# Kernel tuning notes

Hardware: AMD Instinct MI355X
Metric: run time of the kernel (lower is better)

## Reference

```python
import jax, jax.numpy as jnp
import numpy as np

B, H, L, D = 2, 16, 2048, 128


def setup_inputs() -> dict:
    key = jax.random.key(0)
    kq, kk, kv = jax.random.split(key, 3)
    q = jax.random.normal(kq, (B, H, L, D), dtype=jnp.float32)
    k = jax.random.normal(kk, (B, H, L, D), dtype=jnp.float32)
    v = jax.random.normal(kv, (B, H, L, D), dtype=jnp.float32)
    return {"q": q, "k": k, "v": v}


def reference(q, k, v):
    # Causal prefill attention (flash_attn_varlen_func / SDPA is_causal=True path).
    # q, k, v: [B, H, L, D]; scale = 1/sqrt(D) as in the fallback and constructor.
    Lq = q.shape[2]
    Dh = q.shape[3]
    scale = 1.0 / jnp.sqrt(jnp.asarray(Dh, q.dtype))
    scores = jnp.einsum('bhqd,bhkd->bhqk', q, k) * scale  # [B,H,Lq,Lk]
    causal = jnp.tril(jnp.ones((Lq, Lq), dtype=bool))      # [Lq,Lk]
    scores = jnp.where(causal, scores, jnp.finfo(q.dtype).min)
    probs = jax.nn.softmax(scores, axis=-1)
    return jnp.einsum('bhqk,bhkd->bhqd', probs, v)          # [B,H,Lq,D]
```

## Files before the change

kernel.cpp:

```cpp
#include <hip/hip_runtime.h>
#include <hip/hip_bf16.h>
#include <stdint.h>


#define BB 2
#define HH 16
#define LL 2048
#define DD 128

typedef float f32x4 __attribute__((ext_vector_type(4)));
typedef __bf16 bf16x8 __attribute__((ext_vector_type(8)));

union Frag16 {
    uint4    u;
    bf16x8   b;
    uint16_t s[8];
    uint32_t w32[4];
};

__device__ inline uint32_t pk2bf(float x, float y) {
    uint32_t ux = __builtin_bit_cast(uint32_t, x);
    uint32_t uy = __builtin_bit_cast(uint32_t, y);
    ux += 0x7fffu + ((ux >> 16) & 1u);
    uy += 0x7fffu + ((uy >> 16) & 1u);
    return (ux >> 16) | (uy & 0xffff0000u);
}

__device__ inline uint16_t f2bf(float x) {
    uint32_t u = __builtin_bit_cast(uint32_t, x);
    u += 0x7fffu + ((u >> 16) & 1u);
    return (uint16_t)(u >> 16);
}

__global__ __launch_bounds__(256) void conv_all(
    const float* __restrict__ Qg, const float* __restrict__ Kg,
    const float* __restrict__ Vg,
    uint4* __restrict__ Qf, uint4* __restrict__ Kf, uint4* __restrict__ Vf)
{
    const int bid = blockIdx.x;
    const int t   = threadIdx.x;
    if (bid < 4096) {
        const bool isK = bid >= 2048;
        const int  unit = isK ? bid - 2048 : bid;
        const float* src = isK ? Kg : Qg;
        uint4*       dst = isK ? Kf : Qf;
        #pragma unroll
        for (int i = 0; i < 2; ++i) {
            const int local = t + i * 256;
            const int tile  = unit * 2 + (local >> 8);
            const int c     = local & 255;
            const int ds = c >> 6, quad = (c >> 4) & 3, n16 = c & 15;
            const float* p = src + ((size_t)tile * 16 + n16) * DD + ds * 32 + quad * 8;
            float4 a = *(const float4*)p;
            float4 b = *(const float4*)(p + 4);
            Frag16 f;
            f.w32[0] = pk2bf(a.x, a.y); f.w32[1] = pk2bf(a.z, a.w);
            f.w32[2] = pk2bf(b.x, b.y); f.w32[3] = pk2bf(b.z, b.w);
            dst[(size_t)tile * 256 + c] = f.u;
        }
    } else {
        const int g = bid - 4096;
        const int n16 = t & 15, dt = (t >> 4) & 7, quadH = t >> 7;
        #pragma unroll
        for (int qi = 0; qi < 2; ++qi) {
            const int quad = quadH + 2 * qi;
            const float* base = Vg + ((size_t)g * 32 + quad * 8) * DD + dt * 16 + n16;
            float v[8];
            #pragma unroll
            for (int j = 0; j < 8; ++j) v[j] = base[(size_t)j * DD];
            Frag16 f;
            f.w32[0] = pk2bf(v[0], v[1]); f.w32[1] = pk2bf(v[2], v[3]);
            f.w32[2] = pk2bf(v[4], v[5]); f.w32[3] = pk2bf(v[6], v[7]);
            Vf[(size_t)g * 512 + dt * 64 + quad * 16 + n16] = f.u;
        }
    }
}

__global__ __launch_bounds__(256, 2) void fa_main(
    const uint4* __restrict__ Qf, const uint4* __restrict__ Kf,
    const uint4* __restrict__ Vf, float* __restrict__ Og)
{
    __shared__ __align__(16) uint16_t Plds[4][16 * 72];

    const int tid  = threadIdx.x;
    const int lane = tid & 63;
    const int w    = tid >> 6;
    const int n16  = lane & 15;
    const int quad = lane >> 4;

    const int i    = blockIdx.x;
    const int xcd  = i & 7;
    const int rest = i >> 3;
    const int bh   = xcd * 4 + (rest >> 4);
    const int pair = rest & 15;

    constexpr float kC   = 0.08838834764831845f * 1.4426950408889634f;
    constexpr float kOff = -16.0f * 1.4426950408889634f;

    const uint4* kpb = Kf + (size_t)(bh * 128) * 256 + lane;
    const uint4* vpb = Vf + (size_t)(bh * 64) * 512 + lane;
    float* Oh = Og + (size_t)bh * LL * DD;

    #pragma unroll
    for (int phase = 0; phase < 2; ++phase) {
        const int qtile  = phase ? pair : 31 - pair;
        const int q0     = qtile * 64;
        const int q_base = q0 + w * 16;

        Frag16 qf[4];
        {
            const uint4* qp = Qf + ((size_t)(bh * 128 + (q_base >> 4)) * 256) + lane;
            #pragma unroll
            for (int ds = 0; ds < 4; ++ds) qf[ds].u = qp[ds * 64];
        }

        f32x4 oacc[8];
        #pragma unroll
        for (int dt = 0; dt < 8; ++dt) oacc[dt] = (f32x4)0.0f;
        float lpart = 0.0f;

        const int ntiles = (q0 >> 6) + 1;

        for (int t = 0; t < ntiles; ++t) {
            const int kv0 = t << 6;
            const uint4* kp = kpb + (size_t)(kv0 >> 4) * 256;
            const uint4* vp = vpb + (size_t)(kv0 >> 5) * 512;

            f32x4 sacc[4] = {(f32x4)0.0f, (f32x4)0.0f, (f32x4)0.0f, (f32x4)0.0f};
            {
                Frag16 kf[2][4];
                #pragma unroll
                for (int kt = 0; kt < 2; ++kt)
                    #pragma unroll
                    for (int ds = 0; ds < 4; ++ds) kf[kt][ds].u = kp[kt * 256 + ds * 64];
                #pragma unroll
                for (int ds = 0; ds < 4; ++ds) {
                    sacc[0] = __builtin_amdgcn_mfma_f32_16x16x32_bf16(kf[0][ds].b, qf[ds].b, sacc[0], 0, 0, 0);
                    sacc[1] = __builtin_amdgcn_mfma_f32_16x16x32_bf16(kf[1][ds].b, qf[ds].b, sacc[1], 0, 0, 0);
                }
                #pragma unroll
                for (int kt = 0; kt < 2; ++kt)
                    #pragma unroll
                    for (int ds = 0; ds < 4; ++ds) kf[kt][ds].u = kp[(kt + 2) * 256 + ds * 64];
                #pragma unroll
                for (int ds = 0; ds < 4; ++ds) {
                    sacc[2] = __builtin_amdgcn_mfma_f32_16x16x32_bf16(kf[0][ds].b, qf[ds].b, sacc[2], 0, 0, 0);
                    sacc[3] = __builtin_amdgcn_mfma_f32_16x16x32_bf16(kf[1][ds].b, qf[ds].b, sacc[3], 0, 0, 0);
                }
            }

            Frag16 vf[2][8];
            #pragma unroll
            for (int h = 0; h < 2; ++h)
                #pragma unroll
                for (int dt = 0; dt < 8; ++dt) vf[h][dt].u = vp[h * 512 + dt * 64];

            if (kv0 + 63 > q_base) {
                const int qg_ = q_base + n16;
                #pragma unroll
                for (int kt = 0; kt < 4; ++kt) {
                    const int kvg = kv0 + kt * 16 + quad * 4;
                    #pragma unroll
                    for (int r = 0; r < 4; ++r)
                        if (kvg + r > qg_) sacc[kt][r] = -1e30f;
                }
            }

            #pragma unroll
            for (int kt = 0; kt < 4; ++kt) {
                float p0 = exp2f(fmaf(sacc[kt][0], kC, kOff));
                float p1 = exp2f(fmaf(sacc[kt][1], kC, kOff));
                float p2 = exp2f(fmaf(sacc[kt][2], kC, kOff));
                float p3 = exp2f(fmaf(sacc[kt][3], kC, kOff));
                lpart += (p0 + p1) + (p2 + p3);
                uint2 pw;
                pw.x = pk2bf(p0, p1);
                pw.y = pk2bf(p2, p3);
                *(uint2*)&Plds[w][n16 * 72 + kt * 16 + quad * 4] = pw;
            }

            #pragma unroll
            for (int h = 0; h < 2; ++h) {
                Frag16 pf;
                pf.u = *(const uint4*)&Plds[w][n16 * 72 + h * 32 + quad * 8];
                #pragma unroll
                for (int dt = 0; dt < 8; ++dt)
                    oacc[dt] = __builtin_amdgcn_mfma_f32_16x16x32_bf16(
                        pf.b, vf[h][dt].b, oacc[dt], 0, 0, 0);
            }
        }

        float lsum = lpart;
        lsum += __shfl_xor(lsum, 16);
        lsum += __shfl_xor(lsum, 32);
        #pragma unroll
        for (int r = 0; r < 4; ++r) {
            const float inv = 1.0f / __shfl(lsum, quad * 4 + r);
            float* orow = Oh + (size_t)(q_base + quad * 4 + r) * DD + n16;
            #pragma unroll
            for (int dt = 0; dt < 8; ++dt)
                orow[dt * 16] = oacc[dt][r] * inv;
        }
    }
}

__global__ __launch_bounds__(256) void fa_fallback(
    const float* __restrict__ Qg, const float* __restrict__ Kg,
    const float* __restrict__ Vg, float* __restrict__ Og)
{
    __shared__ uint4 Klds[32 * 16];
    __shared__ uint4 Vlds[128 * 4];
    __shared__ __align__(16) uint16_t Plds[4][32 * 40];

    const int tid  = threadIdx.x;
    const int lane = tid & 63;
    const int w    = tid >> 6;
    const int n16  = lane & 15;
    const int quad = lane >> 4;

    const int bh     = blockIdx.y;
    const int q0     = (gridDim.x - 1 - blockIdx.x) * 128;
    const int q_base = q0 + w * 32;

    const size_t base = (size_t)bh * LL * DD;
    const float* Qh = Qg + base;
    const float* Kh = Kg + base;
    const float* Vh = Vg + base;
    float*       Oh = Og + base;

    constexpr float kC = 0.08838834764831845f * 1.4426950408889634f;

    Frag16 qf[2][4];
    #pragma unroll
    for (int qt = 0; qt < 2; ++qt) {
        const float* qrow = Qh + (size_t)(q_base + qt * 16 + n16) * DD;
        #pragma unroll
        for (int ds = 0; ds < 4; ++ds) {
            const int d0 = ds * 32 + quad * 8;
            float4 a = *(const float4*)(qrow + d0);
            float4 b = *(const float4*)(qrow + d0 + 4);
            Frag16 f;
            f.s[0] = f2bf(a.x); f.s[1] = f2bf(a.y); f.s[2] = f2bf(a.z); f.s[3] = f2bf(a.w);
            f.s[4] = f2bf(b.x); f.s[5] = f2bf(b.y); f.s[6] = f2bf(b.z); f.s[7] = f2bf(b.w);
            qf[qt][ds] = f;
        }
    }

    f32x4 oacc[2][8];
    #pragma unroll
    for (int qt = 0; qt < 2; ++qt)
        #pragma unroll
        for (int dt = 0; dt < 8; ++dt) oacc[qt][dt] = (f32x4)0.0f;
    float mrow[2] = {-1e30f, -1e30f};
    float lrow[2] = {0.0f, 0.0f};

    const int ntiles = q0 / 32 + 4;

    for (int t = 0; t < ntiles; ++t) {
        const int kv0 = t * 32;
        __syncthreads();
        #pragma unroll
        for (int iu = 0; iu < 2; ++iu) {
            const int cid = tid + iu * 256;
            const int r = cid >> 4, c = cid & 15;
            const float* src = Kh + (size_t)(kv0 + r) * DD + c * 8;
            float4 a = *(const float4*)src;
            float4 b = *(const float4*)(src + 4);
            Frag16 f;
            f.s[0] = f2bf(a.x); f.s[1] = f2bf(a.y); f.s[2] = f2bf(a.z); f.s[3] = f2bf(a.w);
            f.s[4] = f2bf(b.x); f.s[5] = f2bf(b.y); f.s[6] = f2bf(b.z); f.s[7] = f2bf(b.w);
            Klds[r * 16 + (c ^ (r & 7))] = f.u;
        }
        #pragma unroll
        for (int iu = 0; iu < 2; ++iu) {
            const int cid = tid + iu * 256;
            const int d = cid >> 2, ch = cid & 3;
            const float* src = Vh + (size_t)(kv0 + ch * 8) * DD + d;
            Frag16 f;
            #pragma unroll
            for (int j = 0; j < 8; ++j) f.s[j] = f2bf(src[(size_t)j * DD]);
            Vlds[d * 4 + (ch ^ ((d >> 1) & 3))] = f.u;
        }
        __syncthreads();

        if (kv0 > q_base + 31) continue;

        f32x4 sacc[2][2];
        #pragma unroll
        for (int kt = 0; kt < 2; ++kt)
            #pragma unroll
            for (int qt = 0; qt < 2; ++qt) sacc[kt][qt] = (f32x4)0.0f;

        #pragma unroll
        for (int ds = 0; ds < 4; ++ds) {
            Frag16 kfr[2];
            #pragma unroll
            for (int kt = 0; kt < 2; ++kt) {
                const int r = kt * 16 + n16;
                const int c = ds * 4 + quad;
                kfr[kt].u = Klds[r * 16 + (c ^ (r & 7))];
            }
            #pragma unroll
            for (int kt = 0; kt < 2; ++kt)
                #pragma unroll
                for (int qt = 0; qt < 2; ++qt)
                    sacc[kt][qt] = __builtin_amdgcn_mfma_f32_16x16x32_bf16(
                        kfr[kt].b, qf[qt][ds].b, sacc[kt][qt], 0, 0, 0);
        }

        if (kv0 + 31 > q_base) {
            #pragma unroll
            for (int kt = 0; kt < 2; ++kt) {
                const int kvg = kv0 + kt * 16 + quad * 4;
                #pragma unroll
                for (int qt = 0; qt < 2; ++qt) {
                    const int qg_ = q_base + qt * 16 + n16;
                    #pragma unroll
                    for (int r = 0; r < 4; ++r)
                        if (kvg + r > qg_) sacc[kt][qt][r] = -1e30f;
                }
            }
        }

        #pragma unroll
        for (int qt = 0; qt < 2; ++qt) {
            float mt = sacc[0][qt][0];
            #pragma unroll
            for (int kt = 0; kt < 2; ++kt)
                #pragma unroll
                for (int r = 0; r < 4; ++r) mt = fmaxf(mt, sacc[kt][qt][r]);
            mt = fmaxf(mt, __shfl_xor(mt, 16));
            mt = fmaxf(mt, __shfl_xor(mt, 32));
            const float mnew  = fmaxf(mrow[qt], mt);
            const float alpha = exp2f((mrow[qt] - mnew) * kC);
            mrow[qt] = mnew;

            float ls = 0.0f;
            uint16_t* prow = &Plds[w][(qt * 16 + n16) * 40];
            #pragma unroll
            for (int kt = 0; kt < 2; ++kt)
                #pragma unroll
                for (int r = 0; r < 4; ++r) {
                    const float p = exp2f((sacc[kt][qt][r] - mnew) * kC);
                    ls += p;
                    prow[kt * 16 + quad * 4 + r] = f2bf(p);
                }
            ls += __shfl_xor(ls, 16);
            ls += __shfl_xor(ls, 32);
            lrow[qt] = lrow[qt] * alpha + ls;

            #pragma unroll
            for (int r = 0; r < 4; ++r) {
                const float ar = __shfl(alpha, quad * 4 + r);
                #pragma unroll
                for (int dt = 0; dt < 8; ++dt) oacc[qt][dt][r] *= ar;
            }
        }

        Frag16 pfr[2];
        #pragma unroll
        for (int qt = 0; qt < 2; ++qt)
            pfr[qt].u = *(const uint4*)&Plds[w][(qt * 16 + n16) * 40 + quad * 8];
        #pragma unroll
        for (int dt = 0; dt < 8; ++dt) {
            const int d = dt * 16 + n16;
            Frag16 vfr;
            vfr.u = Vlds[d * 4 + (quad ^ ((d >> 1) & 3))];
            #pragma unroll
            for (int qt = 0; qt < 2; ++qt)
                oacc[qt][dt] = __builtin_amdgcn_mfma_f32_16x16x32_bf16(
                    pfr[qt].b, vfr.b, oacc[qt][dt], 0, 0, 0);
        }
    }

    #pragma unroll
    for (int qt = 0; qt < 2; ++qt) {
        #pragma unroll
        for (int r = 0; r < 4; ++r) {
            const float lr  = __shfl(lrow[qt], quad * 4 + r);
            const float inv = 1.0f / lr;
            const int row = q_base + qt * 16 + quad * 4 + r;
            float* orow = Oh + (size_t)row * DD + n16;
            #pragma unroll
            for (int dt = 0; dt < 8; ++dt)
                orow[dt * 16] = oacc[qt][dt][r] * inv;
        }
    }
}

extern "C" void kernel_launch(void* const* d_in, const int* in_sizes, int n_in,
                              void* d_out, int out_size, void* d_ws, size_t ws_size,
                              hipStream_t stream) {
    const float* q = (const float*)d_in[0];
    const float* k = (const float*)d_in[1];
    const float* v = (const float*)d_in[2];
    float* o = (float*)d_out;

    const size_t TENS = (size_t)BB * HH * LL * DD * 2;
    if (ws_size >= 3 * TENS) {
        uint4* Qf = (uint4*)d_ws;
        uint4* Kf = (uint4*)((char*)d_ws + TENS);
        uint4* Vf = (uint4*)((char*)d_ws + 2 * TENS);
        conv_all<<<dim3(6144), dim3(256), 0, stream>>>(q, k, v, Qf, Kf, Vf);
        fa_main<<<dim3(512), dim3(256), 0, stream>>>(Qf, Kf, Vf, o);
    } else {
        fa_fallback<<<dim3(16, BB * HH), dim3(256), 0, stream>>>(q, k, v, o);
    }
}
```

Measured before the change: 206.1 us.

## Split KV range across warps per 16-row query chunk with LDS reduction

```diff
diff --git a/kernel.cpp b/kernel.cpp
--- a/kernel.cpp
+++ b/kernel.cpp
@@ -76,11 +76,13 @@
     }
 }
 
-__global__ __launch_bounds__(256, 2) void fa_main(
+__global__ __launch_bounds__(256, 4) void fa_main(
     const uint4* __restrict__ Qf, const uint4* __restrict__ Kf,
     const uint4* __restrict__ Vf, float* __restrict__ Og)
 {
     __shared__ __align__(16) uint16_t Plds[4][16 * 72];
+    __shared__ float Olds[3 * 16 * 128];
+    __shared__ float Llds[4 * 16];
 
     const int tid  = threadIdx.x;
     const int lane = tid & 63;
@@ -88,11 +90,12 @@
     const int n16  = lane & 15;
     const int quad = lane >> 4;
 
-    const int i    = blockIdx.x;
-    const int xcd  = i & 7;
-    const int rest = i >> 3;
-    const int bh   = xcd * 4 + (rest >> 4);
-    const int pair = rest & 15;
+    const int i     = blockIdx.x;
+    const int xcd   = i & 7;
+    const int rest  = i >> 3;
+    const int bh    = xcd * 4 + (rest >> 7);
+    const int chunk = 127 - (rest & 127);
+    const int q_base = chunk * 16;
 
     constexpr float kC   = 0.08838834764831845f * 1.4426950408889634f;
     constexpr float kOff = -16.0f * 1.4426950408889634f;
@@ -101,105 +104,119 @@
     const uint4* vpb = Vf + (size_t)(bh * 64) * 512 + lane;
     float* Oh = Og + (size_t)bh * LL * DD;
 
+    Frag16 qf[4];
+    {
+        const uint4* qp = Qf + ((size_t)(bh * 128 + chunk) * 256) + lane;
+        #pragma unroll
+        for (int ds = 0; ds < 4; ++ds) qf[ds].u = qp[ds * 64];
+    }
+
+    f32x4 oacc[8];
     #pragma unroll
-    for (int phase = 0; phase < 2; ++phase) {
-        const int qtile  = phase ? pair : 31 - pair;
-        const int q0     = qtile * 64;
-        const int q_base = q0 + w * 16;
-
-        Frag16 qf[4];
+    for (int dt = 0; dt < 8; ++dt) oacc[dt] = (f32x4)0.0f;
+    float lpart = 0.0f;
+
+    const int ntiles = (q_base >> 6) + 1;
+
+    for (int t = w; t < ntiles; t += 4) {
+        const int kv0 = t << 6;
+        const uint4* kp = kpb + (size_t)(kv0 >> 4) * 256;
+        const uint4* vp = vpb + (size_t)(kv0 >> 5) * 512;
+
+        f32x4 sacc[4] = {(f32x4)0.0f, (f32x4)0.0f, (f32x4)0.0f, (f32x4)0.0f};
         {
-            const uint4* qp = Qf + ((size_t)(bh * 128 + (q_base >> 4)) * 256) + lane;
-            #pragma unroll
-            for (int ds = 0; ds < 4; ++ds) qf[ds].u = qp[ds * 64];
-        }
-
-        f32x4 oacc[8];
-        #pragma unroll
-        for (int dt = 0; dt < 8; ++dt) oacc[dt] = (f32x4)0.0f;
-        float lpart = 0.0f;
-
-        const int ntiles = (q0 >> 6) + 1;
-
-        for (int t = 0; t < ntiles; ++t) {
-            const int kv0 = t << 6;
-            const uint4* kp = kpb + (size_t)(kv0 >> 4) * 256;
-            const uint4* vp = vpb + (size_t)(kv0 >> 5) * 512;
-
-            f32x4 sacc[4] = {(f32x4)0.0f, (f32x4)0.0f, (f32x4)0.0f, (f32x4)0.0f};
-            {
-                Frag16 kf[2][4];
-                #pragma unroll
-                for (int kt = 0; kt < 2; ++kt)
-                    #pragma unroll
-                    for (int ds = 0; ds < 4; ++ds) kf[kt][ds].u = kp[kt * 256 + ds * 64];
-                #pragma unroll
-                for (int ds = 0; ds < 4; ++ds) {
-                    sacc[0] = __builtin_amdgcn_mfma_f32_16x16x32_bf16(kf[0][ds].b, qf[ds].b, sacc[0], 0, 0, 0);
-                    sacc[1] = __builtin_amdgcn_mfma_f32_16x16x32_bf16(kf[1][ds].b, qf[ds].b, sacc[1], 0, 0, 0);
-                }
-                #pragma unroll
-                for (int kt = 0; kt < 2; ++kt)
-                    #pragma unroll
-                    for (int ds = 0; ds < 4; ++ds) kf[kt][ds].u = kp[(kt + 2) * 256 + ds * 64];
-                #pragma unroll
-                for (int ds = 0; ds < 4; ++ds) {
-                    sacc[2] = __builtin_amdgcn_mfma_f32_16x16x32_bf16(kf[0][ds].b, qf[ds].b, sacc[2], 0, 0, 0);
-                    sacc[3] = __builtin_amdgcn_mfma_f32_16x16x32_bf16(kf[1][ds].b, qf[ds].b, sacc[3], 0, 0, 0);
-                }
-            }
-
-            Frag16 vf[2][8];
-            #pragma unroll
-            for (int h = 0; h < 2; ++h)
-                #pragma unroll
-                for (int dt = 0; dt < 8; ++dt) vf[h][dt].u = vp[h * 512 + dt * 64];
-
-            if (kv0 + 63 > q_base) {
-                const int qg_ = q_base + n16;
-                #pragma unroll
-                for (int kt = 0; kt < 4; ++kt) {
-                    const int kvg = kv0 + kt * 16 + quad * 4;
-                    #pragma unroll
-                    for (int r = 0; r < 4; ++r)
-                        if (kvg + r > qg_) sacc[kt][r] = -1e30f;
-                }
-            }
-
+            Frag16 kf[2][4];
+            #pragma unroll
+            for (int kt = 0; kt < 2; ++kt)
+                #pragma unroll
+                for (int ds = 0; ds < 4; ++ds) kf[kt][ds].u = kp[kt * 256 + ds * 64];
+            #pragma unroll
+            for (int ds = 0; ds < 4; ++ds) {
+                sacc[0] = __builtin_amdgcn_mfma_f32_16x16x32_bf16(kf[0][ds].b, qf[ds].b, sacc[0], 0, 0, 0);
+                sacc[1] = __builtin_amdgcn_mfma_f32_16x16x32_bf16(kf[1][ds].b, qf[ds].b, sacc[1], 0, 0, 0);
+            }
+            #pragma unroll
+            for (int kt = 0; kt < 2; ++kt)
+                #pragma unroll
+                for (int ds = 0; ds < 4; ++ds) kf[kt][ds].u = kp[(kt + 2) * 256 + ds * 64];
+            #pragma unroll
+            for (int ds = 0; ds < 4; ++ds) {
+                sacc[2] = __builtin_amdgcn_mfma_f32_16x16x32_bf16(kf[0][ds].b, qf[ds].b, sacc[2], 0, 0, 0);
+                sacc[3] = __builtin_amdgcn_mfma_f32_16x16x32_bf16(kf[1][ds].b, qf[ds].b, sacc[3], 0, 0, 0);
+            }
+        }
+
+        Frag16 vf[2][8];
+        #pragma unroll
+        for (int h = 0; h < 2; ++h)
+            #pragma unroll
+            for (int dt = 0; dt < 8; ++dt) vf[h][dt].u = vp[h * 512 + dt * 64];
+
+        if (kv0 + 63 > q_base) {
+            const int qg_ = q_base + n16;
             #pragma unroll
             for (int kt = 0; kt < 4; ++kt) {
-                float p0 = exp2f(fmaf(sacc[kt][0], kC, kOff));
-                float p1 = exp2f(fmaf(sacc[kt][1], kC, kOff));
-                float p2 = exp2f(fmaf(sacc[kt][2], kC, kOff));
-                float p3 = exp2f(fmaf(sacc[kt][3], kC, kOff));
-                lpart += (p0 + p1) + (p2 + p3);
-                uint2 pw;
-                pw.x = pk2bf(p0, p1);
-                pw.y = pk2bf(p2, p3);
-                *(uint2*)&Plds[w][n16 * 72 + kt * 16 + quad * 4] = pw;
-            }
-
-            #pragma unroll
-            for (int h = 0; h < 2; ++h) {
-                Frag16 pf;
-                pf.u = *(const uint4*)&Plds[w][n16 * 72 + h * 32 + quad * 8];
-                #pragma unroll
-                for (int dt = 0; dt < 8; ++dt)
-                    oacc[dt] = __builtin_amdgcn_mfma_f32_16x16x32_bf16(
-                        pf.b, vf[h][dt].b, oacc[dt], 0, 0, 0);
-            }
-        }
-
-        float lsum = lpart;
-        lsum += __shfl_xor(lsum, 16);
-        lsum += __shfl_xor(lsum, 32);
+                const int kvg = kv0 + kt * 16 + quad * 4;
+                #pragma unroll
+                for (int r = 0; r < 4; ++r)
+                    if (kvg + r > qg_) sacc[kt][r] = -1e30f;
+            }
+        }
+
+        #pragma unroll
+        for (int kt = 0; kt < 4; ++kt) {
+            float p0 = exp2f(fmaf(sacc[kt][0], kC, kOff));
+            float p1 = exp2f(fmaf(sacc[kt][1], kC, kOff));
+            float p2 = exp2f(fmaf(sacc[kt][2], kC, kOff));
+            float p3 = exp2f(fmaf(sacc[kt][3], kC, kOff));
+            lpart += (p0 + p1) + (p2 + p3);
+            uint2 pw;
+            pw.x = pk2bf(p0, p1);
+            pw.y = pk2bf(p2, p3);
+            *(uint2*)&Plds[w][n16 * 72 + kt * 16 + quad * 4] = pw;
+        }
+
+        #pragma unroll
+        for (int h = 0; h < 2; ++h) {
+            Frag16 pf;
+            pf.u = *(const uint4*)&Plds[w][n16 * 72 + h * 32 + quad * 8];
+            #pragma unroll
+            for (int dt = 0; dt < 8; ++dt)
+                oacc[dt] = __builtin_amdgcn_mfma_f32_16x16x32_bf16(
+                    pf.b, vf[h][dt].b, oacc[dt], 0, 0, 0);
+        }
+    }
+
+    float lsum = lpart;
+    lsum += __shfl_xor(lsum, 16);
+    lsum += __shfl_xor(lsum, 32);
+    if (lane < 16) Llds[w * 16 + lane] = lsum;
+
+    if (w > 0) {
+        float* dst = &Olds[(w - 1) * 2048];
         #pragma unroll
         for (int r = 0; r < 4; ++r) {
-            const float inv = 1.0f / __shfl(lsum, quad * 4 + r);
-            float* orow = Oh + (size_t)(q_base + quad * 4 + r) * DD + n16;
+            const int row = quad * 4 + r;
             #pragma unroll
             for (int dt = 0; dt < 8; ++dt)
-                orow[dt * 16] = oacc[dt][r] * inv;
+                dst[row * 128 + dt * 16 + n16] = oacc[dt][r];
+        }
+    }
+    __syncthreads();
+
+    if (w == 0) {
+        #pragma unroll
+        for (int r = 0; r < 4; ++r) {
+            const int row = quad * 4 + r;
+            const float lt = Llds[row] + Llds[16 + row] + Llds[32 + row] + Llds[48 + row];
+            const float inv = 1.0f / lt;
+            float* orow = Oh + (size_t)(q_base + row) * DD + n16;
+            #pragma unroll
+            for (int dt = 0; dt < 8; ++dt) {
+                const int off = row * 128 + dt * 16 + n16;
+                float v = oacc[dt][r] + Olds[off] + Olds[2048 + off] + Olds[4096 + off];
+                orow[dt * 16] = v * inv;
+            }
         }
     }
 }
@@ -402,7 +419,7 @@
         uint4* Kf = (uint4*)((char*)d_ws + TENS);
         uint4* Vf = (uint4*)((char*)d_ws + 2 * TENS);
         conv_all<<<dim3(6144), dim3(256), 0, stream>>>(q, k, v, Qf, Kf, Vf);
-        fa_main<<<dim3(512), dim3(256), 0, stream>>>(Qf, Kf, Vf, o);
+        fa_main<<<dim3(4096), dim3(256), 0, stream>>>(Qf, Kf, Vf, o);
     } else {
         fa_fallback<<<dim3(16, BB * HH), dim3(256), 0, stream>>>(q, k, v, o);
     }
```

After: 328.3 us. 59.3% more time.
